# Performance work log

Hardware: AMD Instinct MI355X
Metric: run time of the kernel (lower is better)

## Reference

```python
import jax, jax.numpy as jnp
import numpy as np

N, E, D, H = 100000, 1600000, 32, 32


def setup_inputs() -> dict:
    key = jax.random.key(0)
    k1, k2, k3, k4 = jax.random.split(key, 4)
    x = jax.random.normal(k1, (N, D), dtype=jnp.float32)
    edge_index = jax.random.randint(k2, (2, E), 0, N, dtype=jnp.int64)
    W1 = jax.random.normal(k3, (D, H), dtype=jnp.float32) * (1.0 / np.sqrt(D))
    b1 = jnp.zeros((H,), dtype=jnp.float32)
    W2 = jax.random.normal(k4, (H, H), dtype=jnp.float32) * (1.0 / np.sqrt(H))
    b2 = jnp.zeros((H,), dtype=jnp.float32)
    return {"x": x, "edge_index": edge_index, "W1": W1, "b1": b1, "W2": W2, "b2": b2}


def _gcn_conv(x, src, dst, norm, W, b, n_nodes):
    # h = x W  ->  gather at src, scale by sym-norm, scatter-add at dst, + bias
    h = x @ W                                   # [N, H]
    msg = h[src] * norm[:, None]                # [E+N, H]
    out = jax.ops.segment_sum(msg, dst, num_segments=n_nodes)
    return out + b


def reference(x, edge_index, W1, b1, W2, b2):
    n = x.shape[0]
    loops = jnp.arange(n, dtype=edge_index.dtype)
    src = jnp.concatenate([edge_index[0], loops])  # source nodes (+ self loops)
    dst = jnp.concatenate([edge_index[1], loops])  # target nodes (+ self loops)
    # symmetric normalization: deg^{-1/2}[src] * deg^{-1/2}[dst] on A + I
    deg = jax.ops.segment_sum(jnp.ones_like(dst, dtype=x.dtype), dst, num_segments=n)
    dis = jnp.where(deg > 0, jax.lax.rsqrt(jnp.maximum(deg, 1e-12)), 0.0)
    norm = dis[src] * dis[dst]
    # layer 1: GCNConv -> ReLU (dropout is identity in eval mode)
    h = jax.nn.relu(_gcn_conv(x, src, dst, norm, W1, b1, n))
    # layer 2
    h = jax.nn.relu(_gcn_conv(h, src, dst, norm, W2, b2, n))
    return h
```

## Files before the change

### kernel.cpp

```cpp
#include <hip/hip_runtime.h>
#include <hip/hip_fp16.h>

#define FEAT 32
#define BIN_NODES 128
#define BIN_SHIFT 7
#define TILE_EDGES 8192
#define BWAVES 16
#define SRC_BITS 20
#define SRC_MASK 0xFFFFF

__device__ __forceinline__ int block_detect_int64(const int* __restrict__ raw32, int* nz) {
    if (threadIdx.x == 0) *nz = 0;
    __syncthreads();
    if (raw32[2 * threadIdx.x + 1] != 0) *nz = 1;
    __syncthreads();
    return (*nz == 0) ? 1 : 0;
}

__device__ __forceinline__ int load_idx(const void* raw, int f, long long i) {
    return f ? (int)((const long long*)raw)[i] : ((const int*)raw)[i];
}

__global__ __launch_bounds__(1024)
void binA_kernel(const void* __restrict__ raw, int* __restrict__ mat, int e, int nb) {
    extern __shared__ int hist[];
    int t = threadIdx.x;
    for (int i = t; i < BWAVES * nb; i += 1024) hist[i] = 0;
    int f = block_detect_int64((const int*)raw, &hist[BWAVES * nb]);
    int w = t >> 6, lane = t & 63;
    long long base = (long long)blockIdx.x * TILE_EDGES;
    int cnt = (int)min((long long)TILE_EDGES, (long long)e - base);
    int* hw = hist + w * nb;
    const int seg = TILE_EDGES / BWAVES;
    int wbeg = w * seg;
    int wend = min(wbeg + seg, cnt);
    for (int i = wbeg + lane; i < wend; i += 64) {
        int d = load_idx(raw, f, (long long)e + base + i);
        atomicAdd(&hw[d >> BIN_SHIFT], 1);
    }
    __syncthreads();
    for (int b = t; b < nb; b += 1024) {
        int s = 0;
#pragma unroll
        for (int w2 = 0; w2 < BWAVES; ++w2) s += hist[w2 * nb + b];
        mat[blockIdx.x * nb + b] = s;
    }
}

__device__ __forceinline__ int l2p(int L, int nb, int nblk) {
    int b = L / nblk;
    int k = L - b * nblk;
    return k * nb + b;
}

__global__ void scan1_kernel(int* __restrict__ mat, int* __restrict__ bsum,
                             int M, int nb, int nblk) {
    __shared__ int sd[256];
    int t = threadIdx.x;
    int L = blockIdx.x * 256 + t;
    int p = 0, v = 0;
    if (L < M) { p = l2p(L, nb, nblk); v = mat[p]; }
    sd[t] = v;
    __syncthreads();
    for (int off = 1; off < 256; off <<= 1) {
        int add = (t >= off) ? sd[t - off] : 0;
        __syncthreads();
        sd[t] += add;
        __syncthreads();
    }
    if (L < M) mat[p] = sd[t] - v;
    if (t == 255) bsum[blockIdx.x] = sd[t];
}

__global__ void scan2_kernel(int* __restrict__ bsum, int nbks) {
    __shared__ int sd[1024];
    int t = threadIdx.x;
    int v = (t < nbks) ? bsum[t] : 0;
    sd[t] = v;
    __syncthreads();
    for (int off = 1; off < 1024; off <<= 1) {
        int add = (t >= off) ? sd[t - off] : 0;
        __syncthreads();
        sd[t] += add;
        __syncthreads();
    }
    if (t < nbks) bsum[t] = sd[t] - v;
}

__global__ __launch_bounds__(1024)
void binC_kernel(const void* __restrict__ raw, const int* __restrict__ mat,
                 const int* __restrict__ bsum, int* __restrict__ packed,
                 int e, int nb, int nblk) {
    extern __shared__ int cur[];
    int t = threadIdx.x;
    int f = block_detect_int64((const int*)raw, &cur[nb]);
    for (int i = t; i < nb; i += 1024)
        cur[i] = mat[blockIdx.x * nb + i] + bsum[(i * nblk + blockIdx.x) >> 8];
    __syncthreads();
    long long base = (long long)blockIdx.x * TILE_EDGES;
    int cnt = (int)min((long long)TILE_EDGES, (long long)e - base);
    for (int i = t; i < cnt; i += 1024) {
        long long ei = base + i;
        int s = load_idx(raw, f, ei);
        int d = load_idx(raw, f, (long long)e + ei);
        int b = d >> BIN_SHIFT;
        int pos = atomicAdd(&cur[b], 1);
        packed[pos] = s | ((d & (BIN_NODES - 1)) << SRC_BITS);
    }
}

__global__ __launch_bounds__(1024)
void degsort_kernel(const int* __restrict__ packed, const int* __restrict__ mat,
                    const int* __restrict__ bsum, float* __restrict__ dis,
                    int* __restrict__ row_start, int* __restrict__ recs,
                    const float* __restrict__ x, const float* __restrict__ W1,
                    __half* __restrict__ h1,
                    int e, int n, int nb, int nblk) {
    __shared__ int cnt[BWAVES][BIN_NODES];
    __shared__ int wcur[BWAVES][BIN_NODES];
    __shared__ int exc[BIN_NODES];
    __shared__ float sdis[BIN_NODES];
    __shared__ float W1l[FEAT * FEAT];
    int b = blockIdx.x, t = threadIdx.x;
    int w = t >> 6;
    for (int i = t; i < BWAVES * BIN_NODES; i += 1024) ((int*)cnt)[i] = 0;
    if (t < FEAT * FEAT) W1l[t] = W1[t];
    __syncthreads();
    int start = mat[b] + bsum[(b * nblk) >> 8];
    int end = (b + 1 < nb) ? (mat[b + 1] + bsum[((b + 1) * nblk) >> 8]) : e;
    for (int i = start + t; i < end; i += 1024)
        atomicAdd(&cnt[w][packed[i] >> SRC_BITS], 1);
    __syncthreads();
    if (t < BIN_NODES) {
        int s = 0;
#pragma unroll
        for (int w2 = 0; w2 < BWAVES; ++w2) s += cnt[w2][t];
        exc[t] = s;
    }
    __syncthreads();
    for (int off = 1; off < BIN_NODES; off <<= 1) {
        int v = 0;
        if (t < BIN_NODES && t >= off) v = exc[t - off];
        __syncthreads();
        if (t < BIN_NODES) exc[t] += v;
        __syncthreads();
    }
    if (t < BIN_NODES) {
        int tot = 0;
#pragma unroll
        for (int w2 = 0; w2 < BWAVES; ++w2) tot += cnt[w2][t];
        int rs = start + exc[t] - tot;
        int run = rs;
#pragma unroll
        for (int w2 = 0; w2 < BWAVES; ++w2) { wcur[w2][t] = run; run += cnt[w2][t]; }
        float dv = rsqrtf((float)tot + 1.0f);
        sdis[t] = dv;
        int node = b * BIN_NODES + t;
        if (node < n) {
            dis[node] = dv;
            row_start[node] = rs;
        }
    }
    if (b == 0 && t == 128) row_start[n] = e;
    __syncthreads();
    for (int i = start + t; i < end; i += 1024) {
        int rec = packed[i];
        int pos = atomicAdd(&wcur[w][rec >> SRC_BITS], 1);
        recs[pos] = rec & SRC_MASK;
    }
    {
        int ln = b * BIN_NODES + (t >> 3);
        if (ln < n) {
            int q = t & 7;
            float4 xv = ((const float4*)x)[(size_t)ln * 8 + q];
            float xr[4] = {xv.x, xv.y, xv.z, xv.w};
            float o[4] = {0.f, 0.f, 0.f, 0.f};
#pragma unroll
            for (int k = 0; k < FEAT; ++k) {
                float xk = __shfl(xr[k & 3], k >> 2, 8);
#pragma unroll
                for (int c = 0; c < 4; ++c)
                    o[c] = fmaf(xk, W1l[k * FEAT + q * 4 + c], o[c]);
            }
            float dn = sdis[t >> 3];
            __half2* hp = (__half2*)&h1[(size_t)ln * FEAT + q * 4];
            hp[0] = __halves2half2(__float2half(dn * o[0]), __float2half(dn * o[1]));
            hp[1] = __halves2half2(__float2half(dn * o[2]), __float2half(dn * o[3]));
        }
    }
}

__global__ __launch_bounds__(256, 6)
void pull_mm_kernel(const int* __restrict__ recs, const int* __restrict__ row_start,
                    const __half* __restrict__ h, const float* __restrict__ dis,
                    const float* __restrict__ bias, const float* __restrict__ W2,
                    __half* __restrict__ h2, int n) {
    __shared__ float Wl[FEAT * FEAT];
    int t = threadIdx.x;
    for (int i = t; i < FEAT * FEAT; i += 256) {
        int k = i >> 5, j = i & 31;
        int col = (j & 24) | ((j + 2 * (k >> 3)) & 7);
        Wl[k * FEAT + col] = W2[i];
    }
    __syncthreads();
    int node = blockIdx.x * 16 + (t >> 4);
    if (node >= n) return;
    int g = t & 15;
    int sub = g >> 2;
    int fb = g & 3;
    int start = row_start[node];
    int deg = row_start[node + 1] - start;
    const float4* h4 = (const float4*)h;
    float s0 = 0, s1 = 0, s2 = 0, s3 = 0, s4 = 0, s5 = 0, s6 = 0, s7 = 0;
    for (int r0 = 0; r0 < deg; r0 += 32) {
#pragma unroll
        for (int w = 0; w < 8; ++w) {
            int r = r0 + w * 4 + sub;
            if (r < deg) {
                int s = recs[start + r];
                float4 v = h4[(size_t)s * 4 + fb];
                const __half2* hp = (const __half2*)&v;
                float2 a = __half22float2(hp[0]);
                float2 b = __half22float2(hp[1]);
                float2 c = __half22float2(hp[2]);
                float2 d = __half22float2(hp[3]);
                s0 += a.x; s1 += a.y; s2 += b.x; s3 += b.y;
                s4 += c.x; s5 += c.y; s6 += d.x; s7 += d.y;
            }
        }
    }
#pragma unroll
    for (int m = 4; m <= 8; m <<= 1) {
        s0 += __shfl_xor(s0, m, 64); s1 += __shfl_xor(s1, m, 64);
        s2 += __shfl_xor(s2, m, 64); s3 += __shfl_xor(s3, m, 64);
        s4 += __shfl_xor(s4, m, 64); s5 += __shfl_xor(s5, m, 64);
        s6 += __shfl_xor(s6, m, 64); s7 += __shfl_xor(s7, m, 64);
    }
    float dn = dis[node];
    float4 hv = h4[(size_t)node * 4 + fb];
    const __half2* hp = (const __half2*)&hv;
    float2 a = __half22float2(hp[0]);
    float2 b = __half22float2(hp[1]);
    float2 c = __half22float2(hp[2]);
    float2 d = __half22float2(hp[3]);
    const float4* bv4 = (const float4*)bias;
    float4 b0 = bv4[fb * 2], b1 = bv4[fb * 2 + 1];
    float o[8];
    o[0] = fmaxf(fmaf(dn, s0 + a.x, b0.x), 0.0f);
    o[1] = fmaxf(fmaf(dn, s1 + a.y, b0.y), 0.0f);
    o[2] = fmaxf(fmaf(dn, s2 + b.x, b0.z), 0.0f);
    o[3] = fmaxf(fmaf(dn, s3 + b.y, b0.w), 0.0f);
    o[4] = fmaxf(fmaf(dn, s4 + c.x, b1.x), 0.0f);
    o[5] = fmaxf(fmaf(dn, s5 + c.y, b1.y), 0.0f);
    o[6] = fmaxf(fmaf(dn, s6 + d.x, b1.z), 0.0f);
    o[7] = fmaxf(fmaf(dn, s7 + d.y, b1.w), 0.0f);
    float part[8] = {0.f, 0.f, 0.f, 0.f, 0.f, 0.f, 0.f, 0.f};
    const float* wrow = &Wl[(fb * 8) * FEAT + sub * 8];
#pragma unroll
    for (int cc = 0; cc < 8; ++cc) {
#pragma unroll
        for (int c2 = 0; c2 < 8; ++c2)
            part[c2] = fmaf(o[cc], wrow[cc * FEAT + ((c2 + 2 * fb) & 7)], part[c2]);
    }
#pragma unroll
    for (int m = 1; m <= 2; m <<= 1) {
        part[0] += __shfl_xor(part[0], m, 64); part[1] += __shfl_xor(part[1], m, 64);
        part[2] += __shfl_xor(part[2], m, 64); part[3] += __shfl_xor(part[3], m, 64);
        part[4] += __shfl_xor(part[4], m, 64); part[5] += __shfl_xor(part[5], m, 64);
        part[6] += __shfl_xor(part[6], m, 64); part[7] += __shfl_xor(part[7], m, 64);
    }
    if (fb == 0) {
        __half2 p0 = __halves2half2(__float2half(dn * part[0]), __float2half(dn * part[1]));
        __half2 p1 = __halves2half2(__float2half(dn * part[2]), __float2half(dn * part[3]));
        __half2 p2 = __halves2half2(__float2half(dn * part[4]), __float2half(dn * part[5]));
        __half2 p3 = __halves2half2(__float2half(dn * part[6]), __float2half(dn * part[7]));
        float4 pk;
        ((__half2*)&pk)[0] = p0; ((__half2*)&pk)[1] = p1;
        ((__half2*)&pk)[2] = p2; ((__half2*)&pk)[3] = p3;
        ((float4*)h2)[(size_t)node * 4 + sub] = pk;
    }
}

__global__ __launch_bounds__(256, 6)
void pull_kernel(const int* __restrict__ recs, const int* __restrict__ row_start,
                 const __half* __restrict__ h, const float* __restrict__ dis,
                 const float* __restrict__ bias, float* __restrict__ out, int n) {
    int t = threadIdx.x;
    int node = blockIdx.x * 16 + (t >> 4);
    if (node >= n) return;
    int g = t & 15;
    int sub = g >> 2;
    int fb = g & 3;
    int start = row_start[node];
    int deg = row_start[node + 1] - start;
    const float4* h4 = (const float4*)h;
    float s0 = 0, s1 = 0, s2 = 0, s3 = 0, s4 = 0, s5 = 0, s6 = 0, s7 = 0;
    for (int r0 = 0; r0 < deg; r0 += 32) {
#pragma unroll
        for (int w = 0; w < 8; ++w) {
            int r = r0 + w * 4 + sub;
            if (r < deg) {
                int s = recs[start + r];
                float4 v = h4[(size_t)s * 4 + fb];
                const __half2* hp = (const __half2*)&v;
                float2 a = __half22float2(hp[0]);
                float2 b = __half22float2(hp[1]);
                float2 c = __half22float2(hp[2]);
                float2 d = __half22float2(hp[3]);
                s0 += a.x; s1 += a.y; s2 += b.x; s3 += b.y;
                s4 += c.x; s5 += c.y; s6 += d.x; s7 += d.y;
            }
        }
    }
#pragma unroll
    for (int m = 4; m <= 8; m <<= 1) {
        s0 += __shfl_xor(s0, m, 64); s1 += __shfl_xor(s1, m, 64);
        s2 += __shfl_xor(s2, m, 64); s3 += __shfl_xor(s3, m, 64);
        s4 += __shfl_xor(s4, m, 64); s5 += __shfl_xor(s5, m, 64);
        s6 += __shfl_xor(s6, m, 64); s7 += __shfl_xor(s7, m, 64);
    }
    if (sub == 0) {
        float dn = dis[node];
        float4 hv = h4[(size_t)node * 4 + fb];
        const __half2* hp = (const __half2*)&hv;
        float2 a = __half22float2(hp[0]);
        float2 b = __half22float2(hp[1]);
        float2 c = __half22float2(hp[2]);
        float2 d = __half22float2(hp[3]);
        const float4* bv4 = (const float4*)bias;
        float4 b0 = bv4[fb * 2], b1 = bv4[fb * 2 + 1];
        float4 o0, o1;
        o0.x = fmaxf(fmaf(dn, s0 + a.x, b0.x), 0.0f);
        o0.y = fmaxf(fmaf(dn, s1 + a.y, b0.y), 0.0f);
        o0.z = fmaxf(fmaf(dn, s2 + b.x, b0.z), 0.0f);
        o0.w = fmaxf(fmaf(dn, s3 + b.y, b0.w), 0.0f);
        o1.x = fmaxf(fmaf(dn, s4 + c.x, b1.x), 0.0f);
        o1.y = fmaxf(fmaf(dn, s5 + c.y, b1.y), 0.0f);
        o1.z = fmaxf(fmaf(dn, s6 + d.x, b1.z), 0.0f);
        o1.w = fmaxf(fmaf(dn, s7 + d.y, b1.w), 0.0f);
        ((float4*)out)[(size_t)node * 8 + fb * 2] = o0;
        ((float4*)out)[(size_t)node * 8 + fb * 2 + 1] = o1;
    }
}

extern "C" void kernel_launch(void* const* d_in, const int* in_sizes, int n_in,
                              void* d_out, int out_size, void* d_ws, size_t ws_size,
                              hipStream_t stream) {
    const float* x = (const float*)d_in[0];
    const void* eidx_raw = d_in[1];
    const float* W1 = (const float*)d_in[2];
    const float* b1 = (const float*)d_in[3];
    const float* W2 = (const float*)d_in[4];
    const float* b2 = (const float*)d_in[5];
    float* out = (float*)d_out;

    const int n = in_sizes[0] / FEAT;
    const int e = in_sizes[1] / 2;
    const int nb = (n + BIN_NODES - 1) / BIN_NODES;
    const int nblk = (e + TILE_EDGES - 1) / TILE_EDGES;
    const int M = nb * nblk;
    const int nbks = (M + 255) / 256;

    char* ws = (char*)d_ws;
    size_t off = 0;
    auto alloc = [&](size_t bytes) { char* p = ws + off; off = (off + bytes + 255) & ~(size_t)255; return p; };
    int*    mat       = (int*)   alloc((size_t)M * 4);
    int*    bsum      = (int*)   alloc((size_t)nbks * 4);
    float*  dis       = (float*) alloc((size_t)n * 4);
    int*    row_start = (int*)   alloc((size_t)(n + 1) * 4);
    int*    recs      = (int*)   alloc((size_t)e * 4);
    __half* h1        = (__half*)alloc((size_t)n * FEAT * 2);
    __half* h2        = (__half*)alloc((size_t)(n * FEAT * 2 > e * 4 ? (size_t)n * FEAT * 2 : (size_t)e * 4));
    int*    packed    = (int*)h2;

    const size_t ldsA = (size_t)(BWAVES * nb + 1) * 4;
    const size_t ldsC = (size_t)(nb + 1) * 4;
    const int gNode = (n + 15) / 16;

    binA_kernel<<<nblk, 1024, ldsA, stream>>>(eidx_raw, mat, e, nb);
    scan1_kernel<<<nbks, 256, 0, stream>>>(mat, bsum, M, nb, nblk);
    scan2_kernel<<<1, 1024, 0, stream>>>(bsum, nbks);
    binC_kernel<<<nblk, 1024, ldsC, stream>>>(eidx_raw, mat, bsum, packed, e, nb, nblk);
    degsort_kernel<<<nb, 1024, 0, stream>>>(packed, mat, bsum, dis, row_start,
                                            recs, x, W1, h1, e, n, nb, nblk);

    pull_mm_kernel<<<gNode, 256, 0, stream>>>(recs, row_start, h1, dis, b1, W2, h2, n);
    pull_kernel<<<gNode, 256, 0, stream>>>(recs, row_start, h2, dis, b2, out, n);
}
```

Before: 182.5 us.

## Replace binned two-pass edge sort with global atomic CSR build

Drops the tile/bin histogram pipeline (binA, binC, degsort) in favour of a direct global-atomic degree count, a per-node scan, a node kernel that computes dis, row offsets, cursors and h1, and a global-atomic scatter of source ids into CSR order. This removes the intermediate packed buffer and one full pass over the edges. In exchange, the scatter writes to random locations using global atomics instead of LDS-local atomics, and neighbour order within each row becomes nondeterministic.

```diff
diff --git a/kernel.cpp b/kernel.cpp
--- a/kernel.cpp
+++ b/kernel.cpp
@@ -2,17 +2,14 @@
 #include <hip/hip_fp16.h>
 
 #define FEAT 32
-#define BIN_NODES 128
-#define BIN_SHIFT 7
-#define TILE_EDGES 8192
-#define BWAVES 16
-#define SRC_BITS 20
-#define SRC_MASK 0xFFFFF
-
-__device__ __forceinline__ int block_detect_int64(const int* __restrict__ raw32, int* nz) {
-    if (threadIdx.x == 0) *nz = 0;
-    __syncthreads();
-    if (raw32[2 * threadIdx.x + 1] != 0) *nz = 1;
+
+__device__ __forceinline__ int detect_int64_256(const int* __restrict__ raw32, int* nz) {
+    int t = threadIdx.x;
+    if (t == 0) *nz = 0;
+    __syncthreads();
+#pragma unroll
+    for (int j = 0; j < 4; ++j)
+        if (raw32[2 * (t + 256 * j) + 1] != 0) *nz = 1;
     __syncthreads();
     return (*nz == 0) ? 1 : 0;
 }
@@ -21,45 +18,20 @@
     return f ? (int)((const long long*)raw)[i] : ((const int*)raw)[i];
 }
 
-__global__ __launch_bounds__(1024)
-void binA_kernel(const void* __restrict__ raw, int* __restrict__ mat, int e, int nb) {
-    extern __shared__ int hist[];
-    int t = threadIdx.x;
-    for (int i = t; i < BWAVES * nb; i += 1024) hist[i] = 0;
-    int f = block_detect_int64((const int*)raw, &hist[BWAVES * nb]);
-    int w = t >> 6, lane = t & 63;
-    long long base = (long long)blockIdx.x * TILE_EDGES;
-    int cnt = (int)min((long long)TILE_EDGES, (long long)e - base);
-    int* hw = hist + w * nb;
-    const int seg = TILE_EDGES / BWAVES;
-    int wbeg = w * seg;
-    int wend = min(wbeg + seg, cnt);
-    for (int i = wbeg + lane; i < wend; i += 64) {
-        int d = load_idx(raw, f, (long long)e + base + i);
-        atomicAdd(&hw[d >> BIN_SHIFT], 1);
-    }
-    __syncthreads();
-    for (int b = t; b < nb; b += 1024) {
-        int s = 0;
-#pragma unroll
-        for (int w2 = 0; w2 < BWAVES; ++w2) s += hist[w2 * nb + b];
-        mat[blockIdx.x * nb + b] = s;
-    }
-}
-
-__device__ __forceinline__ int l2p(int L, int nb, int nblk) {
-    int b = L / nblk;
-    int k = L - b * nblk;
-    return k * nb + b;
-}
-
-__global__ void scan1_kernel(int* __restrict__ mat, int* __restrict__ bsum,
-                             int M, int nb, int nblk) {
+__global__ __launch_bounds__(256)
+void deg_kernel(const void* __restrict__ raw, int* __restrict__ deg, int e) {
+    __shared__ int nz;
+    int f = detect_int64_256((const int*)raw, &nz);
+    int stride = gridDim.x * 256;
+    for (long long i = (long long)blockIdx.x * 256 + threadIdx.x; i < e; i += stride)
+        atomicAdd(&deg[load_idx(raw, f, (long long)e + i)], 1);
+}
+
+__global__ void scan1_kernel(int* __restrict__ mat, int* __restrict__ bsum, int n) {
     __shared__ int sd[256];
     int t = threadIdx.x;
     int L = blockIdx.x * 256 + t;
-    int p = 0, v = 0;
-    if (L < M) { p = l2p(L, nb, nblk); v = mat[p]; }
+    int v = (L < n) ? mat[L] : 0;
     sd[t] = v;
     __syncthreads();
     for (int off = 1; off < 256; off <<= 1) {
@@ -68,7 +40,7 @@
         sd[t] += add;
         __syncthreads();
     }
-    if (L < M) mat[p] = sd[t] - v;
+    if (L < n) mat[L] = sd[t] - v;
     if (t == 255) bsum[blockIdx.x] = sd[t];
 }
 
@@ -87,106 +59,49 @@
     if (t < nbks) bsum[t] = sd[t] - v;
 }
 
-__global__ __launch_bounds__(1024)
-void binC_kernel(const void* __restrict__ raw, const int* __restrict__ mat,
-                 const int* __restrict__ bsum, int* __restrict__ packed,
-                 int e, int nb, int nblk) {
-    extern __shared__ int cur[];
-    int t = threadIdx.x;
-    int f = block_detect_int64((const int*)raw, &cur[nb]);
-    for (int i = t; i < nb; i += 1024)
-        cur[i] = mat[blockIdx.x * nb + i] + bsum[(i * nblk + blockIdx.x) >> 8];
-    __syncthreads();
-    long long base = (long long)blockIdx.x * TILE_EDGES;
-    int cnt = (int)min((long long)TILE_EDGES, (long long)e - base);
-    for (int i = t; i < cnt; i += 1024) {
-        long long ei = base + i;
-        int s = load_idx(raw, f, ei);
-        int d = load_idx(raw, f, (long long)e + ei);
-        int b = d >> BIN_SHIFT;
-        int pos = atomicAdd(&cur[b], 1);
-        packed[pos] = s | ((d & (BIN_NODES - 1)) << SRC_BITS);
-    }
-}
-
-__global__ __launch_bounds__(1024)
-void degsort_kernel(const int* __restrict__ packed, const int* __restrict__ mat,
-                    const int* __restrict__ bsum, float* __restrict__ dis,
-                    int* __restrict__ row_start, int* __restrict__ recs,
-                    const float* __restrict__ x, const float* __restrict__ W1,
-                    __half* __restrict__ h1,
-                    int e, int n, int nb, int nblk) {
-    __shared__ int cnt[BWAVES][BIN_NODES];
-    __shared__ int wcur[BWAVES][BIN_NODES];
-    __shared__ int exc[BIN_NODES];
-    __shared__ float sdis[BIN_NODES];
+__global__ __launch_bounds__(256)
+void node_kernel(const int* __restrict__ mat, const int* __restrict__ bsum,
+                 const float* __restrict__ x, const float* __restrict__ W1,
+                 float* __restrict__ dis, int* __restrict__ row_start,
+                 int* __restrict__ cursor, __half* __restrict__ h1, int n, int e) {
     __shared__ float W1l[FEAT * FEAT];
-    int b = blockIdx.x, t = threadIdx.x;
-    int w = t >> 6;
-    for (int i = t; i < BWAVES * BIN_NODES; i += 1024) ((int*)cnt)[i] = 0;
-    if (t < FEAT * FEAT) W1l[t] = W1[t];
-    __syncthreads();
-    int start = mat[b] + bsum[(b * nblk) >> 8];
-    int end = (b + 1 < nb) ? (mat[b + 1] + bsum[((b + 1) * nblk) >> 8]) : e;
-    for (int i = start + t; i < end; i += 1024)
-        atomicAdd(&cnt[w][packed[i] >> SRC_BITS], 1);
-    __syncthreads();
-    if (t < BIN_NODES) {
-        int s = 0;
-#pragma unroll
-        for (int w2 = 0; w2 < BWAVES; ++w2) s += cnt[w2][t];
-        exc[t] = s;
-    }
-    __syncthreads();
-    for (int off = 1; off < BIN_NODES; off <<= 1) {
-        int v = 0;
-        if (t < BIN_NODES && t >= off) v = exc[t - off];
-        __syncthreads();
-        if (t < BIN_NODES) exc[t] += v;
-        __syncthreads();
-    }
-    if (t < BIN_NODES) {
-        int tot = 0;
-#pragma unroll
-        for (int w2 = 0; w2 < BWAVES; ++w2) tot += cnt[w2][t];
-        int rs = start + exc[t] - tot;
-        int run = rs;
-#pragma unroll
-        for (int w2 = 0; w2 < BWAVES; ++w2) { wcur[w2][t] = run; run += cnt[w2][t]; }
-        float dv = rsqrtf((float)tot + 1.0f);
-        sdis[t] = dv;
-        int node = b * BIN_NODES + t;
-        if (node < n) {
-            dis[node] = dv;
-            row_start[node] = rs;
-        }
-    }
-    if (b == 0 && t == 128) row_start[n] = e;
-    __syncthreads();
-    for (int i = start + t; i < end; i += 1024) {
-        int rec = packed[i];
-        int pos = atomicAdd(&wcur[w][rec >> SRC_BITS], 1);
-        recs[pos] = rec & SRC_MASK;
-    }
-    {
-        int ln = b * BIN_NODES + (t >> 3);
-        if (ln < n) {
-            int q = t & 7;
-            float4 xv = ((const float4*)x)[(size_t)ln * 8 + q];
-            float xr[4] = {xv.x, xv.y, xv.z, xv.w};
-            float o[4] = {0.f, 0.f, 0.f, 0.f};
-#pragma unroll
-            for (int k = 0; k < FEAT; ++k) {
-                float xk = __shfl(xr[k & 3], k >> 2, 8);
-#pragma unroll
-                for (int c = 0; c < 4; ++c)
-                    o[c] = fmaf(xk, W1l[k * FEAT + q * 4 + c], o[c]);
-            }
-            float dn = sdis[t >> 3];
-            __half2* hp = (__half2*)&h1[(size_t)ln * FEAT + q * 4];
-            hp[0] = __halves2half2(__float2half(dn * o[0]), __float2half(dn * o[1]));
-            hp[1] = __halves2half2(__float2half(dn * o[2]), __float2half(dn * o[3]));
-        }
+    int t = threadIdx.x;
+    for (int i = t; i < FEAT * FEAT; i += 256) W1l[i] = W1[i];
+    __syncthreads();
+    if (blockIdx.x == 0 && t == 0) row_start[n] = e;
+    int node = blockIdx.x * 32 + (t >> 3);
+    if (node >= n) return;
+    int q = t & 7;
+    int rs = mat[node] + bsum[node >> 8];
+    int end = (node + 1 < n) ? (mat[node + 1] + bsum[(node + 1) >> 8]) : e;
+    float dv = rsqrtf((float)(end - rs) + 1.0f);
+    if (q == 0) { dis[node] = dv; row_start[node] = rs; cursor[node] = rs; }
+    float4 xv = ((const float4*)x)[(size_t)node * 8 + q];
+    float xr[4] = {xv.x, xv.y, xv.z, xv.w};
+    float o[4] = {0.f, 0.f, 0.f, 0.f};
+#pragma unroll
+    for (int k = 0; k < FEAT; ++k) {
+        float xk = __shfl(xr[k & 3], k >> 2, 8);
+#pragma unroll
+        for (int c = 0; c < 4; ++c)
+            o[c] = fmaf(xk, W1l[k * FEAT + q * 4 + c], o[c]);
+    }
+    __half2* hp = (__half2*)&h1[(size_t)node * FEAT + q * 4];
+    hp[0] = __halves2half2(__float2half(dv * o[0]), __float2half(dv * o[1]));
+    hp[1] = __halves2half2(__float2half(dv * o[2]), __float2half(dv * o[3]));
+}
+
+__global__ __launch_bounds__(256)
+void scatter_kernel(const void* __restrict__ raw, int* __restrict__ cursor,
+                    int* __restrict__ recs, int e) {
+    __shared__ int nz;
+    int f = detect_int64_256((const int*)raw, &nz);
+    int stride = gridDim.x * 256;
+    for (long long i = (long long)blockIdx.x * 256 + threadIdx.x; i < e; i += stride) {
+        int s = load_idx(raw, f, i);
+        int d = load_idx(raw, f, (long long)e + i);
+        int pos = atomicAdd(&cursor[d], 1);
+        recs[pos] = s;
     }
 }
 
@@ -356,33 +271,29 @@
 
     const int n = in_sizes[0] / FEAT;
     const int e = in_sizes[1] / 2;
-    const int nb = (n + BIN_NODES - 1) / BIN_NODES;
-    const int nblk = (e + TILE_EDGES - 1) / TILE_EDGES;
-    const int M = nb * nblk;
-    const int nbks = (M + 255) / 256;
+    const int nbks = (n + 255) / 256;
 
     char* ws = (char*)d_ws;
     size_t off = 0;
     auto alloc = [&](size_t bytes) { char* p = ws + off; off = (off + bytes + 255) & ~(size_t)255; return p; };
-    int*    mat       = (int*)   alloc((size_t)M * 4);
+    int*    mat       = (int*)   alloc((size_t)n * 4);
     int*    bsum      = (int*)   alloc((size_t)nbks * 4);
     float*  dis       = (float*) alloc((size_t)n * 4);
     int*    row_start = (int*)   alloc((size_t)(n + 1) * 4);
+    int*    cursor    = (int*)   alloc((size_t)n * 4);
     int*    recs      = (int*)   alloc((size_t)e * 4);
     __half* h1        = (__half*)alloc((size_t)n * FEAT * 2);
-    __half* h2        = (__half*)alloc((size_t)(n * FEAT * 2 > e * 4 ? (size_t)n * FEAT * 2 : (size_t)e * 4));
-    int*    packed    = (int*)h2;
-
-    const size_t ldsA = (size_t)(BWAVES * nb + 1) * 4;
-    const size_t ldsC = (size_t)(nb + 1) * 4;
+    __half* h2        = (__half*)alloc((size_t)n * FEAT * 2);
+
     const int gNode = (n + 15) / 16;
 
-    binA_kernel<<<nblk, 1024, ldsA, stream>>>(eidx_raw, mat, e, nb);
-    scan1_kernel<<<nbks, 256, 0, stream>>>(mat, bsum, M, nb, nblk);
+    hipMemsetAsync(mat, 0, (size_t)n * 4, stream);
+    deg_kernel<<<2048, 256, 0, stream>>>(eidx_raw, mat, e);
+    scan1_kernel<<<nbks, 256, 0, stream>>>(mat, bsum, n);
     scan2_kernel<<<1, 1024, 0, stream>>>(bsum, nbks);
-    binC_kernel<<<nblk, 1024, ldsC, stream>>>(eidx_raw, mat, bsum, packed, e, nb, nblk);
-    degsort_kernel<<<nb, 1024, 0, stream>>>(packed, mat, bsum, dis, row_start,
-                                            recs, x, W1, h1, e, n, nb, nblk);
+    node_kernel<<<(n + 31) / 32, 256, 0, stream>>>(mat, bsum, x, W1, dis,
+                                                   row_start, cursor, h1, n, e);
+    scatter_kernel<<<2048, 256, 0, stream>>>(eidx_raw, cursor, recs, e);
 
     pull_mm_kernel<<<gNode, 256, 0, stream>>>(recs, row_start, h1, dis, b1, W2, h2, n);
     pull_kernel<<<gNode, 256, 0, stream>>>(recs, row_start, h2, dis, b2, out, n);
```

Result: slower. 363.2 us (+99.0%).
